# Kernel optimization log

Hardware: AMD Instinct MI355X
Metric: run time of the kernel (lower is better)

## Reference

```python
import jax, jax.numpy as jnp
import numpy as np

N = 100000
E = 1600000
F_IN = 128
H = 128
NUM_GRAPHS = 512
EPS = 1e-5


def setup_inputs() -> dict:
    key = jax.random.key(0)
    ks = jax.random.split(key, 16)
    x = jax.random.normal(ks[0], (N, F_IN), dtype=jnp.float32)
    edge_index = jax.random.randint(ks[1], (2, E), 0, N, dtype=jnp.int32)
    batch = jnp.sort(jax.random.randint(ks[2], (N,), 0, NUM_GRAPHS, dtype=jnp.int32))
    def lin(k, fi, fo):
        s = 1.0 / np.sqrt(fi)
        return jax.random.uniform(k, (fi, fo), jnp.float32, -s, s)
    return {
        "x": x, "edge_index": edge_index, "batch": batch,
        "W1": lin(ks[3], F_IN, H), "b1": jnp.zeros((H,), jnp.float32),
        "g1": jnp.ones((H,), jnp.float32), "beta1": jnp.zeros((H,), jnp.float32),
        "W2": lin(ks[4], H, H), "b2": jnp.zeros((H,), jnp.float32),
        "g2": jnp.ones((H,), jnp.float32), "beta2": jnp.zeros((H,), jnp.float32),
        "W3": lin(ks[5], H, H), "b3": jnp.zeros((H,), jnp.float32),
        "g3": jnp.ones((H,), jnp.float32), "beta3": jnp.zeros((H,), jnp.float32),
        "Wl": lin(ks[6], H, 1), "bl": jnp.zeros((1,), jnp.float32),
    }


def _layer_norm(x, g, b):
    mu = jnp.mean(x, axis=-1, keepdims=True)
    var = jnp.mean((x - mu) ** 2, axis=-1, keepdims=True)
    return (x - mu) * jax.lax.rsqrt(var + EPS) * g + b


def _gcn_conv(x, W, b, src, dst, dinv):
    # GCNConv: D^{-1/2}(A+I)D^{-1/2} X W + b, deg includes self-loops
    h = x @ W                                   # [N,H]
    enorm = dinv[src] * dinv[dst]               # [E]
    agg = jax.ops.segment_sum(h[src] * enorm[:, None], dst, num_segments=N)
    agg = agg + h * (dinv * dinv)[:, None]      # self-loop contribution
    return agg + b


def reference(x, edge_index, batch, W1, b1, g1, beta1, W2, b2, g2, beta2,
              W3, b3, g3, beta3, Wl, bl):
    src, dst = edge_index[0], edge_index[1]
    deg = 1.0 + jax.ops.segment_sum(jnp.ones((E,), jnp.float32), dst, num_segments=N)
    dinv = jax.lax.rsqrt(deg)
    h = jax.nn.relu(_layer_norm(_gcn_conv(x, W1, b1, src, dst, dinv), g1, beta1))
    h = jax.nn.relu(_layer_norm(_gcn_conv(h, W2, b2, src, dst, dinv), g2, beta2))
    h = jax.nn.relu(_layer_norm(_gcn_conv(h, W3, b3, src, dst, dinv), g3, beta3))
    # global mean pool over graphs
    sums = jax.ops.segment_sum(h, batch, num_segments=NUM_GRAPHS)
    cnts = jax.ops.segment_sum(jnp.ones((N,), jnp.float32), batch, num_segments=NUM_GRAPHS)
    pooled = sums / jnp.maximum(cnts, 1.0)[:, None]
    return pooled @ Wl + bl                     # [NUM_GRAPHS, 1]
```

## Files before the change

### kernel.cpp

```cpp
#include <hip/hip_runtime.h>
#include <hip/hip_bf16.h>
#include <math.h>

#define N_NODES    100000
#define N_EDGES    1600000
#define FDIM       128
#define NUM_GRAPHS 512
#define EPS        1e-5f
#define PADN       100096

#define B_WPK   192

#define NBUCK   196
#define CAPA    9216
#define EB_CHUNK 2048
#define BIN_BLOCKS ((N_EDGES + EB_CHUNK - 1) / EB_CHUNK)
#define SEGSH   14
#define SEGN    8

typedef __attribute__((ext_vector_type(8))) __bf16 bf16x8;
typedef __attribute__((ext_vector_type(4))) float  f32x4;

__device__ __forceinline__ unsigned short f2bf(float f) {
    unsigned u = __builtin_bit_cast(unsigned, f);
    u += 0x7FFF + ((u >> 16) & 1);
    return (unsigned short)(u >> 16);
}

__device__ __forceinline__ void dec4(unsigned dw, float* o) {
    auto lo = __builtin_amdgcn_cvt_pk_f32_fp8(dw, false);
    auto hi = __builtin_amdgcn_cvt_pk_f32_fp8(dw, true);
    o[0] = lo[0]; o[1] = lo[1]; o[2] = hi[0]; o[3] = hi[1];
}

__device__ __forceinline__ void acc16(uint4 v, float* a) {
    float d[16];
    dec4(v.x, &d[0]); dec4(v.y, &d[4]); dec4(v.z, &d[8]); dec4(v.w, &d[12]);
#pragma unroll
    for (int f = 0; f < 16; f++) a[f] += d[f];
}

__device__ __forceinline__ void agg_core_f(const unsigned char* __restrict__ h8,
                                           const int* __restrict__ offs,
                                           const int* __restrict__ csr_src,
                                           float di, int i, int sl,
                                           const float* __restrict__ bias,
                                           const float* __restrict__ gamma,
                                           const float* __restrict__ beta,
                                           float* r) {
    size_t lofs16 = (size_t)sl * 16;
    float a[16];
    {
        uint4 v = *(const uint4*)(h8 + (size_t)i * 128 + lofs16);
        float d[16];
        dec4(v.x, &d[0]); dec4(v.y, &d[4]); dec4(v.z, &d[8]); dec4(v.w, &d[12]);
#pragma unroll
        for (int f = 0; f < 16; f++) a[f] = d[f];
    }

    int eBeg = offs[i], eEnd = offs[i + 1];
    int e = eBeg;
    int s0, s1, s2, s3;
    if (e + 4 <= eEnd) {
        s0 = csr_src[e + 0]; s1 = csr_src[e + 1];
        s2 = csr_src[e + 2]; s3 = csr_src[e + 3];
    }
    for (; e + 8 <= eEnd; e += 4) {
        uint4 v0 = *(const uint4*)(h8 + (size_t)s0 * 128 + lofs16);
        uint4 v1 = *(const uint4*)(h8 + (size_t)s1 * 128 + lofs16);
        uint4 v2 = *(const uint4*)(h8 + (size_t)s2 * 128 + lofs16);
        uint4 v3 = *(const uint4*)(h8 + (size_t)s3 * 128 + lofs16);
        s0 = csr_src[e + 4]; s1 = csr_src[e + 5];
        s2 = csr_src[e + 6]; s3 = csr_src[e + 7];
        acc16(v0, a); acc16(v1, a); acc16(v2, a); acc16(v3, a);
    }
    if (e + 4 <= eEnd) {
        uint4 v0 = *(const uint4*)(h8 + (size_t)s0 * 128 + lofs16);
        uint4 v1 = *(const uint4*)(h8 + (size_t)s1 * 128 + lofs16);
        uint4 v2 = *(const uint4*)(h8 + (size_t)s2 * 128 + lofs16);
        uint4 v3 = *(const uint4*)(h8 + (size_t)s3 * 128 + lofs16);
        acc16(v0, a); acc16(v1, a); acc16(v2, a); acc16(v3, a);
        e += 4;
    }
    for (; e < eEnd; ++e) {
        int s = csr_src[e];
        uint4 v = *(const uint4*)(h8 + (size_t)s * 128 + lofs16);
        acc16(v, a);
    }

    float4 b0 = *(const float4*)(bias + sl * 16);
    float4 b1 = *(const float4*)(bias + sl * 16 + 4);
    float4 b2 = *(const float4*)(bias + sl * 16 + 8);
    float4 b3 = *(const float4*)(bias + sl * 16 + 12);
    a[0]  = fmaf(a[0],  di, b0.x); a[1]  = fmaf(a[1],  di, b0.y);
    a[2]  = fmaf(a[2],  di, b0.z); a[3]  = fmaf(a[3],  di, b0.w);
    a[4]  = fmaf(a[4],  di, b1.x); a[5]  = fmaf(a[5],  di, b1.y);
    a[6]  = fmaf(a[6],  di, b1.z); a[7]  = fmaf(a[7],  di, b1.w);
    a[8]  = fmaf(a[8],  di, b2.x); a[9]  = fmaf(a[9],  di, b2.y);
    a[10] = fmaf(a[10], di, b2.z); a[11] = fmaf(a[11], di, b2.w);
    a[12] = fmaf(a[12], di, b3.x); a[13] = fmaf(a[13], di, b3.y);
    a[14] = fmaf(a[14], di, b3.z); a[15] = fmaf(a[15], di, b3.w);

    float s1v = 0.f, s2v = 0.f;
#pragma unroll
    for (int f = 0; f < 16; f++) { s1v += a[f]; s2v += a[f] * a[f]; }
#pragma unroll
    for (int off = 1; off < 8; off <<= 1) {
        s1v += __shfl_xor(s1v, off);
        s2v += __shfl_xor(s2v, off);
    }
    float mu   = s1v * (1.0f / 128.0f);
    float var  = s2v * (1.0f / 128.0f) - mu * mu;
    float rstd = rsqrtf(var + EPS);

    float4 g0 = *(const float4*)(gamma + sl * 16);
    float4 g1 = *(const float4*)(gamma + sl * 16 + 4);
    float4 g2 = *(const float4*)(gamma + sl * 16 + 8);
    float4 g3 = *(const float4*)(gamma + sl * 16 + 12);
    float4 e0v = *(const float4*)(beta + sl * 16);
    float4 e1v = *(const float4*)(beta + sl * 16 + 4);
    float4 e2v = *(const float4*)(beta + sl * 16 + 8);
    float4 e3v = *(const float4*)(beta + sl * 16 + 12);
    float g[16]  = {g0.x,g0.y,g0.z,g0.w, g1.x,g1.y,g1.z,g1.w,
                    g2.x,g2.y,g2.z,g2.w, g3.x,g3.y,g3.z,g3.w};
    float be[16] = {e0v.x,e0v.y,e0v.z,e0v.w, e1v.x,e1v.y,e1v.z,e1v.w,
                    e2v.x,e2v.y,e2v.z,e2v.w, e3v.x,e3v.y,e3v.z,e3v.w};

#pragma unroll
    for (int f = 0; f < 16; f++)
        r[f] = fmaxf((a[f] - mu) * rstd * g[f] + be[f], 0.f);
}


__global__ __launch_bounds__(256) void k_pre(const int* __restrict__ src,
                                             const int* __restrict__ dst,
                                             int* __restrict__ bcur,
                                             unsigned* __restrict__ binned,
                                             const float* __restrict__ W1,
                                             const float* __restrict__ W2,
                                             const float* __restrict__ W3,
                                             unsigned short* __restrict__ wp) {
    __shared__ int hist[NBUCK];
    __shared__ int lbase[NBUCK];
    __shared__ int loff[NBUCK];
    __shared__ unsigned lpack[EB_CHUNK];
    __shared__ unsigned short lbuck[EB_CHUNK];
    int b = blockIdx.x;
    int t = threadIdx.x;
    if (b < BIN_BLOCKS) {
        int e0 = b * EB_CHUNK;
        int nE = min(EB_CHUNK, N_EDGES - e0);

        for (int j = t; j < NBUCK; j += 256) { hist[j] = 0; loff[j] = 0; }
        __syncthreads();

        for (int k = t; k < nE; k += 256) {
            int e  = e0 + k;
            int d  = dst[e];
            int bk = d >> 9;
            lpack[k] = (unsigned)src[e] | ((unsigned)(d & 511) << 17);
            lbuck[k] = (unsigned short)bk;
            atomicAdd(&hist[bk], 1);
        }
        __syncthreads();
        for (int j = t; j < NBUCK; j += 256)
            lbase[j] = atomicAdd(&bcur[j], hist[j]);
        __syncthreads();

        for (int k = t; k < nE; k += 256) {
            int bk = lbuck[k];
            int p  = lbase[bk] + atomicAdd(&loff[bk], 1);
            binned[(size_t)bk * CAPA + p] = lpack[k];
        }
    } else {
        int wb  = b - BIN_BLOCKS;
        int mat = wb >> 6;
        const float* W = (mat == 0) ? W1 : (mat == 1) ? W2 : W3;
        unsigned short* o = wp + (size_t)mat * 16384;
        int idx = (wb & 63) * 256 + t;
        int j  = idx & 7;
        int l  = (idx >> 3) & 63;
        int ct = (idx >> 9) & 7;
        int ks = idx >> 12;
        int k  = ks * 32 + (l >> 4) * 8 + j;
        int c  = ct * 16 + (l & 15);
        o[idx] = f2bf(W[k * 128 + c]);
    }
}


__global__ __launch_bounds__(256) void k_binB(const unsigned* __restrict__ binned,
                                              const int* __restrict__ bcur,
                                              int* __restrict__ offs,
                                              float* __restrict__ dinv,
                                              int* __restrict__ csr_src) {
    __shared__ int smem[512 * SEGN + 256];
    int* cnt2 = smem;
    int* part = smem + 4096;
    int b = blockIdx.x;
    int t = threadIdx.x;
    int nb0 = b * 512;
    int cnt = bcur[b];

    int pv = (t < b) ? bcur[t] : 0;
#pragma unroll
    for (int off = 32; off; off >>= 1) pv += __shfl_down(pv, off);
    if ((t & 63) == 0) part[t >> 6] = pv;
    __syncthreads();
    int seg0 = part[0] + part[1] + part[2] + part[3];
    __syncthreads();

    for (int j = t; j < 512 * SEGN; j += 256) cnt2[j] = 0;
    __syncthreads();

    for (int k = t; k < cnt; k += 256) {
        unsigned v = binned[(size_t)b * CAPA + k];
        atomicAdd(&cnt2[(v >> 17) * SEGN + ((v & 0x1FFFF) >> SEGSH)], 1);
    }
    __syncthreads();

    int base16 = t * 16;
    int lsum[16];
    int run = 0;
#pragma unroll
    for (int q = 0; q < 16; q++) { lsum[q] = run; run += cnt2[base16 + q]; }
    int deg0 = lsum[8];
    int deg1 = run - lsum[8];
    part[t] = run;
    __syncthreads();
    for (int off = 1; off < 256; off <<= 1) {
        int y = 0;
        if (t >= off) y = part[t - off];
        __syncthreads();
        if (t >= off) part[t] += y;
        __syncthreads();
    }
    int excl = part[t] - run;
#pragma unroll
    for (int q = 0; q < 16; q++) cnt2[base16 + q] = excl + lsum[q];

    {
        int n0 = nb0 + 2 * t;
        if (n0 < N_NODES) {
            offs[n0] = seg0 + excl;
            dinv[n0] = rsqrtf(1.0f + (float)deg0);
        }
        if (n0 + 1 < N_NODES) {
            offs[n0 + 1] = seg0 + excl + lsum[8];
            dinv[n0 + 1] = rsqrtf(1.0f + (float)deg1);
        }
    }
    if (b == NBUCK - 1 && t == 0) offs[N_NODES] = N_EDGES;
    __syncthreads();

    for (int k = t; k < cnt; k += 256) {
        unsigned v = binned[(size_t)b * CAPA + k];
        int p = atomicAdd(&cnt2[(v >> 17) * SEGN + ((v & 0x1FFFF) >> SEGSH)], 1);
        csr_src[seg0 + p] = (int)(v & 0x1FFFF);
    }
}


__global__ __launch_bounds__(256) void k_gemm1(const float* __restrict__ X,
                                               const unsigned short* __restrict__ Wp,
                                               const float* __restrict__ dinv,
                                               unsigned char* __restrict__ C8) {
    int t    = threadIdx.x;
    int lane = t & 63;
    int w    = t >> 6;
    int wc   = w & 1;
    int wr   = w >> 1;
    int rb   = blockIdx.x * 128 + wr * 64 + (lane & 15);
    int koff = (lane >> 4) * 8;

    f32x4 acc[4][4];
#pragma unroll
    for (int c = 0; c < 4; c++)
#pragma unroll
        for (int r = 0; r < 4; r++) acc[c][r] = (f32x4){0.f, 0.f, 0.f, 0.f};

    const bf16x8* Wv = (const bf16x8*)Wp;
#pragma unroll
    for (int ks = 0; ks < 4; ++ks) {
        bf16x8 fw[4], fa[4];
#pragma unroll
        for (int c = 0; c < 4; ++c)
            fw[c] = Wv[(ks * 8 + wc * 4 + c) * 64 + lane];
#pragma unroll
        for (int r = 0; r < 4; ++r) {
            int row = rb + r * 16;
            ushort4 lo = {0,0,0,0}, hi = {0,0,0,0};
            if (row < N_NODES) {
                const float* xp = X + (size_t)row * 128 + ks * 32 + koff;
                float4 xv0 = *(const float4*)xp;
                float4 xv1 = *(const float4*)(xp + 4);
                lo.x = f2bf(xv0.x); lo.y = f2bf(xv0.y);
                lo.z = f2bf(xv0.z); lo.w = f2bf(xv0.w);
                hi.x = f2bf(xv1.x); hi.y = f2bf(xv1.y);
                hi.z = f2bf(xv1.z); hi.w = f2bf(xv1.w);
            }
            uint4 packed = make_uint4(
                (unsigned)lo.x | ((unsigned)lo.y << 16),
                (unsigned)lo.z | ((unsigned)lo.w << 16),
                (unsigned)hi.x | ((unsigned)hi.y << 16),
                (unsigned)hi.z | ((unsigned)hi.w << 16));
            fa[r] = __builtin_bit_cast(bf16x8, packed);
        }
#pragma unroll
        for (int c = 0; c < 4; ++c)
#pragma unroll
            for (int r = 0; r < 4; ++r)
                acc[c][r] = __builtin_amdgcn_mfma_f32_16x16x32_bf16(fw[c], fa[r], acc[c][r], 0, 0, 0);
    }

#pragma unroll
    for (int r = 0; r < 4; ++r) {
        int row = blockIdx.x * 128 + wr * 64 + r * 16 + (lane & 15);
        if (row < N_NODES) {
            float dv = dinv[row];
#pragma unroll
            for (int c = 0; c < 4; ++c) {
                int col = (wc * 4 + c) * 16 + (lane >> 4) * 4;
                unsigned u = __builtin_amdgcn_cvt_pk_fp8_f32(acc[c][r][0] * dv, acc[c][r][1] * dv, 0, false);
                u = (unsigned)__builtin_amdgcn_cvt_pk_fp8_f32(acc[c][r][2] * dv, acc[c][r][3] * dv, (int)u, true);
                *(unsigned*)(C8 + (size_t)row * 128 + col) = u;
            }
        }
    }
}


__global__ __launch_bounds__(256, 4) void k_fused(const unsigned char* __restrict__ h8_in,
                                                  const unsigned short* __restrict__ Wp,
                                                  const float* __restrict__ dinv,
                                                  unsigned char* __restrict__ h8_out,
                                                  const int* __restrict__ offs,
                                                  const int* __restrict__ csr_src,
                                                  const float* __restrict__ bias,
                                                  const float* __restrict__ gamma,
                                                  const float* __restrict__ beta) {
    __shared__ unsigned tile_u[32 * 64];
    int t    = threadIdx.x;
    int lane = t & 63;
    int w    = t >> 6;
    int grp  = lane >> 3;
    int sl   = lane & 7;
    int nt   = w * 8 + grp;
    int i    = blockIdx.x * 32 + nt;

    {
        float r[16];
        agg_core_f(h8_in, offs, csr_src, dinv[i], i, sl, bias, gamma, beta, r);
        unsigned ow[8];
#pragma unroll
        for (int f = 0; f < 8; f++)
            ow[f] = (unsigned)f2bf(r[2 * f]) | ((unsigned)f2bf(r[2 * f + 1]) << 16);
        int rowbase = nt * 64;
        int colu    = sl * 8;
        int swz0 = (colu    ) ^ ((nt & 15) << 2);
        int swz1 = (colu + 4) ^ ((nt & 15) << 2);
        *(uint4*)&tile_u[rowbase + swz0] = make_uint4(ow[0], ow[1], ow[2], ow[3]);
        *(uint4*)&tile_u[rowbase + swz1] = make_uint4(ow[4], ow[5], ow[6], ow[7]);
    }
    __syncthreads();

    f32x4 acc[2][2];
#pragma unroll
    for (int c = 0; c < 2; c++)
#pragma unroll
        for (int r = 0; r < 2; r++) acc[c][r] = (f32x4){0.f, 0.f, 0.f, 0.f};

    const bf16x8* Wv = (const bf16x8*)Wp;
#pragma unroll
    for (int ks = 0; ks < 4; ++ks) {
        bf16x8 fw[2], fa[2];
#pragma unroll
        for (int c = 0; c < 2; ++c)
            fw[c] = Wv[(ks * 8 + w * 2 + c) * 64 + lane];
#pragma unroll
        for (int r = 0; r < 2; ++r) {
            int lr   = r * 16 + (lane & 15);
            int colu = ks * 16 + (lane >> 4) * 4;
            int swz  = colu ^ ((lr & 15) << 2);
            uint4 v = *(const uint4*)&tile_u[lr * 64 + swz];
            fa[r] = __builtin_bit_cast(bf16x8, v);
        }
#pragma unroll
        for (int c = 0; c < 2; ++c)
#pragma unroll
            for (int r = 0; r < 2; ++r)
                acc[c][r] = __builtin_amdgcn_mfma_f32_16x16x32_bf16(fw[c], fa[r], acc[c][r], 0, 0, 0);
    }

#pragma unroll
    for (int r = 0; r < 2; ++r) {
        int row = blockIdx.x * 32 + r * 16 + (lane & 15);
        float dv = dinv[row];
#pragma unroll
        for (int c = 0; c < 2; ++c) {
            int col = (w * 2 + c) * 16 + (lane >> 4) * 4;
            unsigned u = __builtin_amdgcn_cvt_pk_fp8_f32(acc[c][r][0] * dv, acc[c][r][1] * dv, 0, false);
            u = (unsigned)__builtin_amdgcn_cvt_pk_fp8_f32(acc[c][r][2] * dv, acc[c][r][3] * dv, (int)u, true);
            *(unsigned*)(h8_out + (size_t)row * 128 + col) = u;
        }
    }
}


__global__ __launch_bounds__(256) void k_aggpool(const unsigned char* __restrict__ h8,
                                                 const int* __restrict__ offs,
                                                 const int* __restrict__ csr_src,
                                                 const float* __restrict__ dinv,
                                                 const int* __restrict__ batch,
                                                 const float* __restrict__ bias,
                                                 const float* __restrict__ gamma,
                                                 const float* __restrict__ beta,
                                                 float* __restrict__ pooled) {
    __shared__ float wsum[4][128];
    __shared__ int grange[2];
    int t    = threadIdx.x;
    int lane = t & 63;
    int w    = t >> 6;
    int grp  = lane >> 3;
    int sl   = lane & 7;
    int i    = blockIdx.x * 32 + w * 8 + grp;

    float r[16];
    agg_core_f(h8, offs, csr_src, dinv[i], i, sl, bias, gamma, beta, r);

    int bg = batch[i];
    if (t == 0) {
        grange[0] = batch[blockIdx.x * 32];
        grange[1] = batch[blockIdx.x * 32 + 31];
    }
    __syncthreads();
    int g0 = grange[0], g1 = grange[1];

    for (int g = g0; g <= g1; ++g) {
        float v[16];
        bool in = (bg == g);
#pragma unroll
        for (int f = 0; f < 16; f++) v[f] = in ? r[f] : 0.f;
#pragma unroll
        for (int f = 0; f < 16; f++) {
            v[f] += __shfl_xor(v[f], 8);
            v[f] += __shfl_xor(v[f], 16);
            v[f] += __shfl_xor(v[f], 32);
        }
        if (grp == 0) {
#pragma unroll
            for (int f = 0; f < 16; f++) wsum[w][sl * 16 + f] = v[f];
        }
        __syncthreads();
        if (t < 128) {
            float s = wsum[0][t] + wsum[1][t] + wsum[2][t] + wsum[3][t];
            if (s != 0.f) atomicAdd(&pooled[(size_t)g * 128 + t], s);
        }
        __syncthreads();
    }
}


__global__ __launch_bounds__(64) void k_final(const float* __restrict__ pooled,
                                              const int* __restrict__ batch,
                                              const float* __restrict__ Wl,
                                              const float* __restrict__ bl,
                                              float* __restrict__ out) {
    int g = blockIdx.x;
    int lane = threadIdx.x;

    int lo = 0, hi = N_NODES;
    while (lo < hi) { int mid = (lo + hi) >> 1; if (batch[mid] < g) lo = mid + 1; else hi = mid; }
    int s = lo;
    lo = s; hi = N_NODES;
    while (lo < hi) { int mid = (lo + hi) >> 1; if (batch[mid] < g + 1) lo = mid + 1; else hi = mid; }
    int e = lo;

    float inv = 1.0f / fmaxf((float)(e - s), 1.0f);
    float2 p2 = ((const float2*)(pooled + (size_t)g * 128))[lane];
    float p = p2.x * inv * Wl[lane * 2] + p2.y * inv * Wl[lane * 2 + 1];
#pragma unroll
    for (int off = 32; off; off >>= 1) p += __shfl_xor(p, off);
    if (lane == 0) out[g] = p + bl[0];
}


extern "C" void kernel_launch(void* const* d_in, const int* in_sizes, int n_in,
                              void* d_out, int out_size, void* d_ws, size_t ws_size,
                              hipStream_t stream) {
    const float* x     = (const float*)d_in[0];
    const int*   ei    = (const int*)d_in[1];
    const int*   batch = (const int*)d_in[2];
    const float* W1 = (const float*)d_in[3];
    const float* b1 = (const float*)d_in[4];
    const float* g1 = (const float*)d_in[5];
    const float* be1 = (const float*)d_in[6];
    const float* W2 = (const float*)d_in[7];
    const float* b2 = (const float*)d_in[8];
    const float* g2 = (const float*)d_in[9];
    const float* be2 = (const float*)d_in[10];
    const float* W3 = (const float*)d_in[11];
    const float* b3 = (const float*)d_in[12];
    const float* g3 = (const float*)d_in[13];
    const float* be3 = (const float*)d_in[14];
    const float* Wl = (const float*)d_in[15];
    const float* bl = (const float*)d_in[16];

    const int* src = ei;
    const int* dst = ei + N_EDGES;

    char* ws = (char*)d_ws;
    size_t off = 0;
    auto alloc = [&](size_t bytes) -> void* {
        void* p = ws + off;
        off += (bytes + 255) & ~(size_t)255;
        return p;
    };
    unsigned char*  hFa  = (unsigned char*)alloc((size_t)PADN * FDIM);
    unsigned char*  hFb  = (unsigned char*)alloc((size_t)PADN * FDIM);
    unsigned short* wp   = (unsigned short*)alloc((size_t)3 * 16384 * 2);
    float* dinv    = (float*)alloc((size_t)N_NODES * 4);
    int*   offs    = (int*)alloc((size_t)(N_NODES + 1) * 4);
    int*   csr_src = (int*)alloc((size_t)N_EDGES * 4);
    unsigned* binned = (unsigned*)alloc((size_t)NBUCK * CAPA * 4);
    int*   bcur    = (int*)alloc(256 * 4);
    float* pooled  = (float*)alloc((size_t)NUM_GRAPHS * FDIM * 4);

    hipMemsetAsync(bcur, 0, 256 * 4, stream);
    hipMemsetAsync(pooled, 0, (size_t)NUM_GRAPHS * FDIM * 4, stream);

    k_pre<<<BIN_BLOCKS + B_WPK, 256, 0, stream>>>(src, dst, bcur, binned,
                                                  W1, W2, W3, wp);
    k_binB<<<NBUCK, 256, 0, stream>>>(binned, bcur, offs, dinv, csr_src);

    int gemm_grid  = PADN / 128;
    int fuse_grid  = N_NODES / 32;

    k_gemm1<<<gemm_grid, 256, 0, stream>>>(x, wp, dinv, hFa);
    k_fused<<<fuse_grid, 256, 0, stream>>>(hFa, wp + 16384, dinv, hFb,
                                           offs, csr_src, b1, g1, be1);
    k_fused<<<fuse_grid, 256, 0, stream>>>(hFb, wp + 32768, dinv, hFa,
                                           offs, csr_src, b2, g2, be2);
    k_aggpool<<<fuse_grid, 256, 0, stream>>>(hFa, offs, csr_src, dinv, batch,
                                             b3, g3, be3, pooled);
    k_final<<<NUM_GRAPHS, 64, 0, stream>>>(pooled, batch, Wl, bl, (float*)d_out);
}
```

Baseline: 235.9 us.

## Pipeline neighbor gathers through LDS ring with async global_load_lds

Replaces the register-based 4-wide unrolled neighbor gather with an 8-deep per-wave ring buffer in shared memory, filled by asynchronous global-to-LDS loads. This keeps more gathers in flight per lane to hide the latency of random accesses. Each wave iterates to the maximum degree among its 8 nodes, and lanes that run out of edges load a zero-filled padding row, which is why the padding rows are now cleared with memsets. The cost is 32 KB of extra shared memory per block, which may lower occupancy, plus wasted loads on wave-level degree imbalance and per-iteration waitcnt stalls.

Result: slower. 329.7 us (+39.8%).

```diff
diff --git a/kernel.cpp b/kernel.cpp
--- a/kernel.cpp
+++ b/kernel.cpp
@@ -17,9 +17,12 @@
 #define BIN_BLOCKS ((N_EDGES + EB_CHUNK - 1) / EB_CHUNK)
 #define SEGSH   14
 #define SEGN    8
+#define RING    8
 
 typedef __attribute__((ext_vector_type(8))) __bf16 bf16x8;
 typedef __attribute__((ext_vector_type(4))) float  f32x4;
+typedef const __attribute__((address_space(1))) unsigned GU;
+typedef __attribute__((address_space(3))) unsigned LU;
 
 __device__ __forceinline__ unsigned short f2bf(float f) {
     unsigned u = __builtin_bit_cast(unsigned, f);
@@ -40,14 +43,16 @@
     for (int f = 0; f < 16; f++) a[f] += d[f];
 }
 
-__device__ __forceinline__ void agg_core_f(const unsigned char* __restrict__ h8,
-                                           const int* __restrict__ offs,
-                                           const int* __restrict__ csr_src,
-                                           float di, int i, int sl,
-                                           const float* __restrict__ bias,
-                                           const float* __restrict__ gamma,
-                                           const float* __restrict__ beta,
-                                           float* r) {
+__device__ __forceinline__ void agg_core_pipe(const unsigned char* __restrict__ h8,
+                                              const int* __restrict__ offs,
+                                              const int* __restrict__ csr_src,
+                                              float di, int i, int lane,
+                                              unsigned* ring,
+                                              const float* __restrict__ bias,
+                                              const float* __restrict__ gamma,
+                                              const float* __restrict__ beta,
+                                              float* r) {
+    int sl = lane & 7;
     size_t lofs16 = (size_t)sl * 16;
     float a[16];
     {
@@ -58,35 +63,33 @@
         for (int f = 0; f < 16; f++) a[f] = d[f];
     }
 
-    int eBeg = offs[i], eEnd = offs[i + 1];
-    int e = eBeg;
-    int s0, s1, s2, s3;
-    if (e + 4 <= eEnd) {
-        s0 = csr_src[e + 0]; s1 = csr_src[e + 1];
-        s2 = csr_src[e + 2]; s3 = csr_src[e + 3];
-    }
-    for (; e + 8 <= eEnd; e += 4) {
-        uint4 v0 = *(const uint4*)(h8 + (size_t)s0 * 128 + lofs16);
-        uint4 v1 = *(const uint4*)(h8 + (size_t)s1 * 128 + lofs16);
-        uint4 v2 = *(const uint4*)(h8 + (size_t)s2 * 128 + lofs16);
-        uint4 v3 = *(const uint4*)(h8 + (size_t)s3 * 128 + lofs16);
-        s0 = csr_src[e + 4]; s1 = csr_src[e + 5];
-        s2 = csr_src[e + 6]; s3 = csr_src[e + 7];
-        acc16(v0, a); acc16(v1, a); acc16(v2, a); acc16(v3, a);
-    }
-    if (e + 4 <= eEnd) {
-        uint4 v0 = *(const uint4*)(h8 + (size_t)s0 * 128 + lofs16);
-        uint4 v1 = *(const uint4*)(h8 + (size_t)s1 * 128 + lofs16);
-        uint4 v2 = *(const uint4*)(h8 + (size_t)s2 * 128 + lofs16);
-        uint4 v3 = *(const uint4*)(h8 + (size_t)s3 * 128 + lofs16);
-        acc16(v0, a); acc16(v1, a); acc16(v2, a); acc16(v3, a);
-        e += 4;
-    }
-    for (; e < eEnd; ++e) {
-        int s = csr_src[e];
-        uint4 v = *(const uint4*)(h8 + (size_t)s * 128 + lofs16);
+    int eBeg = offs[i];
+    int tg   = offs[i + 1] - eBeg;
+    int T = tg;
+    T = max(T, __shfl_xor(T, 8));
+    T = max(T, __shfl_xor(T, 16));
+    T = max(T, __shfl_xor(T, 32));
+
+#pragma unroll
+    for (int k = 0; k < RING; ++k) {
+        int s = N_NODES;
+        if (k < tg) s = csr_src[eBeg + k];
+        GU* gp = (GU*)(h8 + (size_t)s * 128 + lofs16);
+        __builtin_amdgcn_global_load_lds(gp, (LU*)(ring + k * 256), 16, 0, 0);
+    }
+
+    for (int k = 0; k < T; ++k) {
+        asm volatile("s_waitcnt vmcnt(7)" ::: "memory");
+        uint4 v = *(const uint4*)(ring + (k & (RING - 1)) * 256 + lane * 4);
+        asm volatile("s_waitcnt lgkmcnt(0)" ::: "memory");
+        int kk = k + RING;
+        int s = N_NODES;
+        if (kk < tg) s = csr_src[eBeg + kk];
+        GU* gp = (GU*)(h8 + (size_t)s * 128 + lofs16);
+        __builtin_amdgcn_global_load_lds(gp, (LU*)(ring + (kk & (RING - 1)) * 256), 16, 0, 0);
         acc16(v, a);
     }
+    asm volatile("s_waitcnt vmcnt(0)" ::: "memory");
 
     float4 b0 = *(const float4*)(bias + sl * 16);
     float4 b1 = *(const float4*)(bias + sl * 16 + 4);
@@ -339,6 +342,7 @@
                                                   const float* __restrict__ bias,
                                                   const float* __restrict__ gamma,
                                                   const float* __restrict__ beta) {
+    __shared__ unsigned ring[4][RING * 256];
     __shared__ unsigned tile_u[32 * 64];
     int t    = threadIdx.x;
     int lane = t & 63;
@@ -350,7 +354,8 @@
 
     {
         float r[16];
-        agg_core_f(h8_in, offs, csr_src, dinv[i], i, sl, bias, gamma, beta, r);
+        agg_core_pipe(h8_in, offs, csr_src, dinv[i], i, lane, &ring[w][0],
+                      bias, gamma, beta, r);
         unsigned ow[8];
 #pragma unroll
         for (int f = 0; f < 8; f++)
@@ -416,6 +421,7 @@
                                                  const float* __restrict__ gamma,
                                                  const float* __restrict__ beta,
                                                  float* __restrict__ pooled) {
+    __shared__ unsigned ring[4][RING * 256];
     __shared__ float wsum[4][128];
     __shared__ int grange[2];
     int t    = threadIdx.x;
@@ -426,7 +432,8 @@
     int i    = blockIdx.x * 32 + w * 8 + grp;
 
     float r[16];
-    agg_core_f(h8, offs, csr_src, dinv[i], i, sl, bias, gamma, beta, r);
+    agg_core_pipe(h8, offs, csr_src, dinv[i], i, lane, &ring[w][0],
+                  bias, gamma, beta, r);
 
     int bg = batch[i];
     if (t == 0) {
@@ -528,6 +535,8 @@
 
     hipMemsetAsync(bcur, 0, 256 * 4, stream);
     hipMemsetAsync(pooled, 0, (size_t)NUM_GRAPHS * FDIM * 4, stream);
+    hipMemsetAsync(hFa + (size_t)N_NODES * FDIM, 0, (size_t)(PADN - N_NODES) * FDIM, stream);
+    hipMemsetAsync(hFb + (size_t)N_NODES * FDIM, 0, (size_t)(PADN - N_NODES) * FDIM, stream);
 
     k_pre<<<BIN_BLOCKS + B_WPK, 256, 0, stream>>>(src, dst, bcur, binned,
                                                   W1, W2, W3, wp);
```
